# Performance work log

Measured on AMD Instinct MI355X. Metric: run time of the kernel, lower is better.

The kernel has to match this reference:

```python
import jax, jax.numpy as jnp
import numpy as np

F_BINS, T_STEPS, N_ACTIONS = 257, 65536, 256  # STFT bins, frames, codebook size


def setup_inputs() -> dict:
    key = jax.random.key(0)
    k1, k2, k3, k4 = jax.random.split(key, 4)
    x_out = jax.random.normal(k1, (F_BINS, T_STEPS), dtype=jnp.float32)
    x_source = jax.random.normal(k2, (F_BINS, T_STEPS), dtype=jnp.float32)
    x_clean = jax.random.normal(k3, (F_BINS, T_STEPS), dtype=jnp.float32)
    # G is self.G_mat = G_mat.T, i.e. [freq, action]; gains in [0,1)
    G = jax.random.uniform(k4, (F_BINS, N_ACTIONS), dtype=jnp.float32)
    return {"x_out": x_out, "x_source": x_source, "x_clean": x_clean, "G": G}


def reference(x_out, x_source, x_clean, G):
    # sums[t, a] = sum_f (x_clean[f, t] - G[f, a] * x_source[f, t])
    #            = sum_f x_clean[:, t]  -  (x_source^T @ G)[t, a]
    clean_sum = jnp.sum(x_clean, axis=0)                 # [T]
    proj = jnp.einsum('ft,fa->ta', x_source, G)          # [T, A]
    sums = clean_sum[:, None] - proj                     # [T, A]
    A_t = jnp.argmin(sums, axis=1)                       # [T], values in [0, A)
    F, T = x_source.shape
    # Faithful to the original loop: wiener_true[:, a] = G[:, a] for each
    # SELECTED ACTION a (column indexed by action id, not timestep).
    # Duplicate indices write identical values, so scatter-set is well-defined.
    wiener_true = jnp.zeros((F, T), dtype=x_source.dtype).at[:, A_t].set(G[:, A_t])
    true_out = (wiener_true * x_source).T                # [T, F]
    loss = jnp.mean((true_out - x_out.T) ** 2)
    return loss
```

## Files before the change

kernel.cpp:

```cpp
#include <hip/hip_runtime.h>

#define F_BINS  257
#define T_STEPS 65536
#define N_ACT   256
#define TM      256
#define NBLK_G  256
#define NTHR    512
#define XO_PB   16384
#define XO_MAIN (NBLK_G * XO_PB)

typedef float f32x4 __attribute__((ext_vector_type(4)));
typedef short s16x8 __attribute__((ext_vector_type(8)));
typedef unsigned u32x4 __attribute__((ext_vector_type(4)));

#define WS_PART  1024
#define WS_CORR  20480
#define WS_MASK  24576
#define WS_GFRAG 65536

__device__ __forceinline__ unsigned short f2bf_rne(float x) {
  unsigned u = __builtin_bit_cast(unsigned, x);
  return (unsigned short)((u + 0x7FFFu + ((u >> 16) & 1u)) >> 16);
}
__device__ __forceinline__ unsigned pack_bf(float hi, float lo) {
  return __builtin_amdgcn_perm(__builtin_bit_cast(unsigned, hi),
                               __builtin_bit_cast(unsigned, lo), 0x07060302u);
}

__global__ __launch_bounds__(256) void k_prep(const float* __restrict__ G,
                                              unsigned char* __restrict__ gfrag) {
  const int u = blockIdx.x * 256 + threadIdx.x;
  const int lane = u & 63, ng = (u >> 6) & 15, kk = u >> 10;
  const int r16 = lane & 15, g = lane >> 4;
  const int a = ng * 16 + r16;
  unsigned short h[8];
#pragma unroll
  for (int j = 0; j < 8; ++j) {
    const int f = kk * 32 + 8 * g + j;
    h[j] = (f < F_BINS) ? f2bf_rne(G[f * N_ACT + a]) : (unsigned short)0;
  }
  u32x4 w;
#pragma unroll
  for (int i = 0; i < 4; ++i)
    w[i] = (unsigned)h[2 * i] | ((unsigned)h[2 * i + 1] << 16);
  *(u32x4*)(gfrag + (size_t)u * 16) = w;
}

__global__ __launch_bounds__(NTHR, 2) void k_gemm(
    const float* __restrict__ xs, const float4* __restrict__ xo4,
    const unsigned char* __restrict__ gfrag,
    unsigned* __restrict__ maskp, double* __restrict__ partial) {
  const int tid = threadIdx.x, lane = tid & 63, wv = tid >> 6;
  const int g = lane >> 4, r16 = lane & 15;
  const int t0 = blockIdx.x * TM;
  const int tcol = t0 + 32 * wv + 2 * r16;

  __shared__ __align__(16) unsigned char Bb[147456];
  __shared__ unsigned lmask[8];
  __shared__ double sdw[8];
  if (tid < 8) lmask[tid] = 0u;

#define LOADB(slot, kkv)                                                      \
  {                                                                           \
    _Pragma("unroll") for (int j = 0; j < 8; ++j) {                           \
      int f = 32 * (kkv) + 8 * g + j;                                         \
      if ((kkv) == 8) f = f > 256 ? 256 : f;   \
      va[slot][j] = *(const float2*)(xs + (size_t)f * T_STEPS + tcol);        \
    }                                                                         \
  }

  float2 va[4][8];
  LOADB(0, 0) LOADB(1, 1) LOADB(2, 2) LOADB(3, 3)
  __builtin_amdgcn_sched_barrier(0);
#pragma unroll
  for (int i = 0; i < 18; ++i) {
    const int c = 18 * wv + i;
    const unsigned char* src = gfrag + (size_t)c * 1024 + (size_t)lane * 16;
    unsigned char* dst = &Bb[c * 1024];
    __builtin_amdgcn_global_load_lds(
        (const __attribute__((address_space(1))) unsigned*)src,
        (__attribute__((address_space(3))) unsigned*)dst, 16, 0, 0);
  }
  __builtin_amdgcn_sched_barrier(0);

  s16x8 af[9][2];
#pragma unroll
  for (int kk = 0; kk < 9; ++kk) {
    const int b = kk & 3;
    af[kk][0] = __builtin_bit_cast(s16x8, (u32x4){
        pack_bf(va[b][1].x, va[b][0].x), pack_bf(va[b][3].x, va[b][2].x),
        pack_bf(va[b][5].x, va[b][4].x), pack_bf(va[b][7].x, va[b][6].x)});
    af[kk][1] = __builtin_bit_cast(s16x8, (u32x4){
        pack_bf(va[b][1].y, va[b][0].y), pack_bf(va[b][3].y, va[b][2].y),
        pack_bf(va[b][5].y, va[b][4].y), pack_bf(va[b][7].y, va[b][6].y)});
    if (kk + 4 <= 8) LOADB(b, kk + 4)
  }
#undef LOADB

  asm volatile("s_waitcnt vmcnt(0)" ::: "memory");
  __builtin_amdgcn_s_barrier();

  float bv[2][4]; int bc[2][4];
#pragma unroll
  for (int h = 0; h < 2; ++h) {
    f32x4 acc[2][8];
#pragma unroll
    for (int tau = 0; tau < 2; ++tau)
#pragma unroll
      for (int n = 0; n < 8; ++n) acc[tau][n] = (f32x4){0.f, 0.f, 0.f, 0.f};
#pragma unroll
    for (int kk = 0; kk < 9; ++kk) {
      const unsigned char* bp = &Bb[((kk * 16 + 8 * h) * 64 + lane) * 16];
#pragma unroll
      for (int n = 0; n < 8; ++n) {
        const s16x8 bfr = *(const s16x8*)(bp + n * 1024);
        acc[0][n] = __builtin_amdgcn_mfma_f32_16x16x32_bf16(
            af[kk][0], bfr, acc[0][n], 0, 0, 0);
        acc[1][n] = __builtin_amdgcn_mfma_f32_16x16x32_bf16(
            af[kk][1], bfr, acc[1][n], 0, 0, 0);
      }
    }
#pragma unroll
    for (int n = 0; n < 8; ++n) {
      const int c = 128 * h + 16 * n + r16;
#pragma unroll
      for (int tau = 0; tau < 2; ++tau)
#pragma unroll
        for (int q = 0; q < 4; ++q) {
          const float v = acc[tau][n][q];
          if (h == 0 && n == 0) { bv[tau][q] = v; bc[tau][q] = c; }
          else if (v > bv[tau][q]) { bv[tau][q] = v; bc[tau][q] = c; }
        }
    }
  }

  const float4* xop = xo4 + (size_t)blockIdx.x * XO_PB + tid;
  float4 xv[2][8];
#pragma unroll
  for (int j = 0; j < 8; ++j) xv[0][j] = xop[j * 512];
  float4 wrem = (float4){0.f, 0.f, 0.f, 0.f};
  if (tid < 64) wrem = xo4[XO_MAIN + (size_t)blockIdx.x * 64 + tid];

#pragma unroll
  for (int m = 1; m <= 8; m <<= 1) {
#pragma unroll
    for (int tau = 0; tau < 2; ++tau)
#pragma unroll
      for (int q = 0; q < 4; ++q) {
        const float ov = __shfl_xor(bv[tau][q], m);
        const int   oc = __shfl_xor(bc[tau][q], m);
        if (ov > bv[tau][q] || (ov == bv[tau][q] && oc < bc[tau][q])) {
          bv[tau][q] = ov; bc[tau][q] = oc;
        }
      }
  }
  if (r16 == 0) {
#pragma unroll
    for (int tau = 0; tau < 2; ++tau)
#pragma unroll
      for (int q = 0; q < 4; ++q)
        atomicOr(&lmask[bc[tau][q] >> 5], 1u << (bc[tau][q] & 31));
  }
  __syncthreads();
  if (tid < 8) maskp[blockIdx.x * 8 + tid] = lmask[tid];

  double ds = 0.0;
#pragma unroll
  for (int r = 0; r < 4; ++r) {
    if (r + 1 < 4) {
#pragma unroll
      for (int j = 0; j < 8; ++j)
        xv[(r + 1) & 1][j] = xop[(size_t)(r + 1) * 4096 + j * 512];
    }
    const float4* xc = xv[r & 1];
    float fs = 0.f;
#pragma unroll
    for (int j = 0; j < 8; ++j) {
      fs = fmaf(xc[j].x, xc[j].x, fs); fs = fmaf(xc[j].y, xc[j].y, fs);
      fs = fmaf(xc[j].z, xc[j].z, fs); fs = fmaf(xc[j].w, xc[j].w, fs);
    }
    ds += (double)fs;
  }
  {
    float fs = 0.f;
    fs = fmaf(wrem.x, wrem.x, fs); fs = fmaf(wrem.y, wrem.y, fs);
    fs = fmaf(wrem.z, wrem.z, fs); fs = fmaf(wrem.w, wrem.w, fs);
    ds += (double)fs;
  }
#pragma unroll
  for (int off = 32; off; off >>= 1) ds += __shfl_down(ds, off);
  if (lane == 0) sdw[wv] = ds;
  __syncthreads();
  if (tid == 0) {
    double s = 0.0;
#pragma unroll
    for (int w = 0; w < 8; ++w) s += sdw[w];
    partial[blockIdx.x] = s;
  }
}

__global__ __launch_bounds__(256) void k_corr(
    const float* __restrict__ xs, const float* __restrict__ xo,
    const float* __restrict__ G, const unsigned* __restrict__ maskp,
    double* __restrict__ corrp) {
  __shared__ unsigned m8[8];
  const int tid = threadIdx.x;
  if (tid < 8) m8[tid] = 0u;
  __syncthreads();
  unsigned m = 0;
  for (int b = tid >> 3; b < NBLK_G; b += 32) m |= maskp[b * 8 + (tid & 7)];
  atomicOr(&m8[tid & 7], m);
  __syncthreads();
  const int f = blockIdx.x, a = tid;
  const bool sel = (m8[a >> 5] >> (a & 31)) & 1u;
  const float gv  = G[f * N_ACT + a];
  const float xsv = xs[(size_t)f * T_STEPS + a];
  const float xov = xo[(size_t)f * T_STEPS + a];
  const float gx  = gv * xsv;
  double acc = sel ? (double)(gx * (gx - 2.f * xov)) : 0.0;
#pragma unroll
  for (int off = 32; off; off >>= 1) acc += __shfl_down(acc, off);
  __shared__ double sdc[4];
  if ((tid & 63) == 0) sdc[tid >> 6] = acc;
  __syncthreads();
  if (tid == 0) corrp[f] = sdc[0] + sdc[1] + sdc[2] + sdc[3];
}

__global__ __launch_bounds__(256) void k_final(const double* __restrict__ partial,
                                               const double* __restrict__ corrp,
                                               float* __restrict__ out) {
  const int tid = threadIdx.x;
  double s = partial[tid] + corrp[tid];
  if (tid == 0) s += corrp[256];
#pragma unroll
  for (int off = 32; off; off >>= 1) s += __shfl_down(s, off);
  __shared__ double sd[4];
  if ((tid & 63) == 0) sd[tid >> 6] = s;
  __syncthreads();
  if (tid == 0)
    out[0] = (float)((sd[0] + sd[1] + sd[2] + sd[3]) /
                     ((double)F_BINS * (double)T_STEPS));
}

extern "C" void kernel_launch(void* const* d_in, const int* in_sizes, int n_in,
                              void* d_out, int out_size, void* d_ws, size_t ws_size,
                              hipStream_t stream) {
  const float* x_out    = (const float*)d_in[0];
  const float* x_source = (const float*)d_in[1];
  const float* G        = (const float*)d_in[3];

  char* ws = (char*)d_ws;
  double*        partial = (double*)(ws + WS_PART);
  double*        corrp   = (double*)(ws + WS_CORR);
  unsigned*      maskp   = (unsigned*)(ws + WS_MASK);
  unsigned char* gfrag   = (unsigned char*)(ws + WS_GFRAG);

  k_prep <<<36, 256, 0, stream>>>(G, gfrag);
  k_gemm <<<NBLK_G, NTHR, 0, stream>>>(x_source, (const float4*)x_out,
                                       gfrag, maskp, partial);
  k_corr <<<F_BINS, 256, 0, stream>>>(x_source, x_out, G, maskp, corrp);
  k_final<<<1, 256, 0, stream>>>(partial, corrp, (float*)d_out);
}
```

Baseline: 46.65 us.

## Halve GEMM tile and stage G fragments in two LDS halves

After: 42.00 us, median of 2. 10.0% less time.

```diff
diff --git a/kernel.cpp b/kernel.cpp
--- a/kernel.cpp
+++ b/kernel.cpp
@@ -3,11 +3,10 @@
 #define F_BINS  257
 #define T_STEPS 65536
 #define N_ACT   256
-#define TM      256
-#define NBLK_G  256
-#define NTHR    512
-#define XO_PB   16384
-#define XO_MAIN (NBLK_G * XO_PB)
+#define TM      128
+#define NBLK_G  512
+#define NTHR    256
+#define XO_PB   8224
 
 typedef float f32x4 __attribute__((ext_vector_type(4)));
 typedef short s16x8 __attribute__((ext_vector_type(8)));
@@ -55,11 +54,24 @@
   const int t0 = blockIdx.x * TM;
   const int tcol = t0 + 32 * wv + 2 * r16;
 
-  __shared__ __align__(16) unsigned char Bb[147456];
+  __shared__ __align__(16) unsigned char Bh[73728];
   __shared__ unsigned lmask[8];
-  __shared__ double sdw[8];
+  __shared__ double sdw[4];
   if (tid < 8) lmask[tid] = 0u;
 
+#define STAGE_BH(hv)                                                          \
+  {                                                                           \
+    _Pragma("unroll") for (int idx = 0; idx < 18; ++idx) {                    \
+      const int j = 18 * wv + idx;                      \
+      const int kkc = j >> 3, ic = j & 7;                                     \
+      const unsigned char* src = gfrag +                                      \
+          (size_t)(kkc * 16 + 8 * (hv) + ic) * 1024 + (size_t)lane * 16;      \
+      unsigned char* dst = &Bh[j * 1024];                                     \
+      __builtin_amdgcn_global_load_lds(                                       \
+          (const __attribute__((address_space(1))) unsigned*)src,             \
+          (__attribute__((address_space(3))) unsigned*)dst, 16, 0, 0);        \
+    }                                                                         \
+  }
 #define LOADB(slot, kkv)                                                      \
   {                                                                           \
     _Pragma("unroll") for (int j = 0; j < 8; ++j) {                           \
@@ -72,15 +84,7 @@
   float2 va[4][8];
   LOADB(0, 0) LOADB(1, 1) LOADB(2, 2) LOADB(3, 3)
   __builtin_amdgcn_sched_barrier(0);
-#pragma unroll
-  for (int i = 0; i < 18; ++i) {
-    const int c = 18 * wv + i;
-    const unsigned char* src = gfrag + (size_t)c * 1024 + (size_t)lane * 16;
-    unsigned char* dst = &Bb[c * 1024];
-    __builtin_amdgcn_global_load_lds(
-        (const __attribute__((address_space(1))) unsigned*)src,
-        (__attribute__((address_space(3))) unsigned*)dst, 16, 0, 0);
-  }
+  STAGE_BH(0)
   __builtin_amdgcn_sched_barrier(0);
 
   s16x8 af[9][2];
@@ -97,12 +101,16 @@
   }
 #undef LOADB
 
-  asm volatile("s_waitcnt vmcnt(0)" ::: "memory");
-  __builtin_amdgcn_s_barrier();
+  __syncthreads();
 
   float bv[2][4]; int bc[2][4];
 #pragma unroll
   for (int h = 0; h < 2; ++h) {
+    if (h == 1) {
+      __syncthreads();
+      STAGE_BH(1)
+      __syncthreads();
+    }
     f32x4 acc[2][8];
 #pragma unroll
     for (int tau = 0; tau < 2; ++tau)
@@ -110,7 +118,7 @@
       for (int n = 0; n < 8; ++n) acc[tau][n] = (f32x4){0.f, 0.f, 0.f, 0.f};
 #pragma unroll
     for (int kk = 0; kk < 9; ++kk) {
-      const unsigned char* bp = &Bb[((kk * 16 + 8 * h) * 64 + lane) * 16];
+      const unsigned char* bp = &Bh[(kk * 8 * 64 + lane) * 16];
 #pragma unroll
       for (int n = 0; n < 8; ++n) {
         const s16x8 bfr = *(const s16x8*)(bp + n * 1024);
@@ -133,13 +141,14 @@
         }
     }
   }
+#undef STAGE_BH
 
   const float4* xop = xo4 + (size_t)blockIdx.x * XO_PB + tid;
   float4 xv[2][8];
 #pragma unroll
-  for (int j = 0; j < 8; ++j) xv[0][j] = xop[j * 512];
+  for (int j = 0; j < 8; ++j) xv[0][j] = xop[j * 256];
   float4 wrem = (float4){0.f, 0.f, 0.f, 0.f};
-  if (tid < 64) wrem = xo4[XO_MAIN + (size_t)blockIdx.x * 64 + tid];
+  if (tid < 32) wrem = xo4[(size_t)blockIdx.x * XO_PB + 8192 + tid];
 
 #pragma unroll
   for (int m = 1; m <= 8; m <<= 1) {
@@ -170,7 +179,7 @@
     if (r + 1 < 4) {
 #pragma unroll
       for (int j = 0; j < 8; ++j)
-        xv[(r + 1) & 1][j] = xop[(size_t)(r + 1) * 4096 + j * 512];
+        xv[(r + 1) & 1][j] = xop[(size_t)(r + 1) * 2048 + j * 256];
     }
     const float4* xc = xv[r & 1];
     float fs = 0.f;
@@ -191,12 +200,7 @@
   for (int off = 32; off; off >>= 1) ds += __shfl_down(ds, off);
   if (lane == 0) sdw[wv] = ds;
   __syncthreads();
-  if (tid == 0) {
-    double s = 0.0;
-#pragma unroll
-    for (int w = 0; w < 8; ++w) s += sdw[w];
-    partial[blockIdx.x] = s;
-  }
+  if (tid == 0) partial[blockIdx.x] = sdw[0] + sdw[1] + sdw[2] + sdw[3];
 }
 
 __global__ __launch_bounds__(256) void k_corr(
@@ -230,7 +234,7 @@
                                                const double* __restrict__ corrp,
                                                float* __restrict__ out) {
   const int tid = threadIdx.x;
-  double s = partial[tid] + corrp[tid];
+  double s = partial[tid] + partial[tid + 256] + corrp[tid];
   if (tid == 0) s += corrp[256];
 #pragma unroll
   for (int off = 32; off; off >>= 1) s += __shfl_down(s, off);
```
